# Performance work log

Hardware: AMD Instinct MI355X
Metric: run time of the kernel (lower is better)

## Reference

```python
import jax, jax.numpy as jnp
import numpy as np

ROT_DIM = 32
THETA = 10000.0
HEAD_SIZE = 192


def _rope(t):
    # t: [B, T, D]; rotate first ROT_DIM features with interleaved-pair RoPE
    T = t.shape[1]
    inv_freq = 1.0 / (THETA ** (jnp.arange(0, ROT_DIM, 2, dtype=jnp.float32) / ROT_DIM))  # [16]
    freqs = jnp.arange(T, dtype=jnp.float32)[:, None] * inv_freq[None, :]  # [T,16]
    freqs = jnp.repeat(freqs, 2, axis=-1)  # [T,32], each freq repeated for the pair
    cos = jnp.cos(freqs).astype(t.dtype)
    sin = jnp.sin(freqs).astype(t.dtype)
    x = t[..., :ROT_DIM]
    x1 = x[..., 0::2]
    x2 = x[..., 1::2]
    rot_half = jnp.stack([-x2, x1], axis=-1).reshape(x.shape)  # interleave (-x2, x1)
    rotated = x * cos + rot_half * sin
    return jnp.concatenate([rotated, t[..., ROT_DIM:]], axis=-1)


def setup_inputs() -> dict:
    key = jax.random.key(0)
    k1, k2, k3, k4 = jax.random.split(key, 4)
    B, T, C, H = 64, 512, 768, HEAD_SIZE
    x = jax.random.normal(k1, (B, T, C), dtype=jnp.float32)
    s = 1.0 / np.sqrt(C)
    Wq = jax.random.normal(k2, (C, H), dtype=jnp.float32) * s
    Wk = jax.random.normal(k3, (C, H), dtype=jnp.float32) * s
    Wv = jax.random.normal(k4, (C, H), dtype=jnp.float32) * s
    return {"x": x, "Wq": Wq, "Wk": Wk, "Wv": Wv}


def reference(x, Wq, Wk, Wv):
    B, T, C = x.shape
    q = x @ Wq  # [B,T,H]
    k = x @ Wk
    v = x @ Wv
    q = _rope(q)
    k = _rope(k)
    scale = k.shape[-1] ** -0.5
    scores = jnp.einsum('bqh,bkh->bqk', q, k) * scale  # [B,T,T]
    causal = jnp.tril(jnp.ones((T, T), dtype=bool))
    scores = jnp.where(causal[None, :, :], scores, -jnp.inf)
    weight = jax.nn.softmax(scores, axis=-1)
    # dropout is identity at eval time
    out = jnp.einsum('bqk,bkh->bqh', weight, v)  # [B,T,H]
    return out
```

## Files before the change

### kernel.cpp

```cpp
#include <hip/hip_runtime.h>
#include <cstdint>

typedef __attribute__((ext_vector_type(8))) short short8;
typedef __attribute__((ext_vector_type(4))) float floatx4;

__device__ __forceinline__ unsigned short f2bf(float f) {
  uint32_t u = __builtin_bit_cast(uint32_t, f);
  u += 0x7fffu + ((u >> 16) & 1u);
  return (unsigned short)(u >> 16);
}
__device__ __forceinline__ uint32_t pkbf(float lo, float hi) {
  uint32_t a = __builtin_bit_cast(uint32_t, lo) + 0x8000u;
  uint32_t b = __builtin_bit_cast(uint32_t, hi) + 0x8000u;
  return __builtin_amdgcn_perm(b, a, 0x07060302);
}
__device__ __forceinline__ void gll16(const void* g, void* l) {
  __builtin_amdgcn_global_load_lds(
      (const __attribute__((address_space(1))) unsigned int*)g,
      (__attribute__((address_space(3))) unsigned int*)l, 16, 0, 0);
}

__global__ void prep_w_kernel(const float* __restrict__ Wq,
                              const float* __restrict__ Wk,
                              const float* __restrict__ Wv,
                              unsigned short* __restrict__ Wt) {
  int id = blockIdx.x * 256 + threadIdx.x;
  int bz = id / 18432, rem = id - bz * 18432;
  int kb = rem / 768, s = rem - kb * 768;
  int row = s >> 2, cs = s & 3;
  int c = cs ^ ((row >> 1) & 3);
  const float* W = (bz == 0) ? Wq : (bz == 1) ? Wk : Wv;
  int k0 = kb * 32 + c * 8;
  unsigned short v[8];
#pragma unroll
  for (int e = 0; e < 8; ++e) v[e] = f2bf(W[(size_t)(k0 + e) * 192 + row]);
  uint4 o;
  o.x = v[0] | ((uint32_t)v[1] << 16);
  o.y = v[2] | ((uint32_t)v[3] << 16);
  o.z = v[4] | ((uint32_t)v[5] << 16);
  o.w = v[6] | ((uint32_t)v[7] << 16);
  *(uint4*)(Wt + (size_t)id * 8) = o;
}

__global__ __launch_bounds__(256, 3) void proj_kernel(
    const float* __restrict__ x, const unsigned short* __restrict__ Wt,
    unsigned short* __restrict__ q_ws, unsigned short* __restrict__ k_ws,
    unsigned short* __restrict__ v_ws) {
  __shared__ __align__(16) unsigned short A_lds[3][64 * 32];
  __shared__ __align__(16) unsigned short B_lds[3][192 * 32];
  const int tid = threadIdx.x;
  const int w = tid >> 6, l = tid & 63, quad = l >> 4, ln = l & 15;
  const int wr = w & 1, wc = w >> 1;
  const int m0 = blockIdx.x * 64;
  const int bz = blockIdx.y;

  const int arow = tid >> 2, ac = tid & 3;
  const int aslot = ((ac ^ ((arow >> 1) & 3)) << 4);
  const float* xp = x + (size_t)(m0 + arow) * 768 + ac * 8;
  const unsigned short* wimg = Wt + (size_t)bz * 18432 * 8;

  const int fq = ((quad ^ ((ln >> 1) & 3)) << 4);

  floatx4 acc[2][6];
#pragma unroll
  for (int mi = 0; mi < 2; ++mi)
#pragma unroll
    for (int nj = 0; nj < 6; ++nj) acc[mi][nj] = floatx4{0.f, 0.f, 0.f, 0.f};

  float4 ax0, ay0, ax1, ay1, ax2, ay2;

#define LOADA(S, K0)                               \
  do {                                             \
    ax##S = *(const float4*)(xp + (K0));           \
    ay##S = *(const float4*)(xp + (K0) + 4);       \
  } while (0)
#define STAGEA(S, AB)                                             \
  do {                                                            \
    uint4 ap;                                                     \
    ap.x = pkbf(ax##S.x, ax##S.y);                                \
    ap.y = pkbf(ax##S.z, ax##S.w);                                \
    ap.z = pkbf(ay##S.x, ay##S.y);                                \
    ap.w = pkbf(ay##S.z, ay##S.w);                                \
    *(uint4*)((char*)&A_lds[AB][0] + arow * 64 + aslot) = ap;     \
  } while (0)
#define DMAB(KB1, BB)                                             \
  do {                                                            \
    const unsigned short* src = wimg + (size_t)(KB1)*6144;        \
    char* dstb = (char*)&B_lds[BB][0];                            \
    gll16(src + tid * 8, dstb + tid * 16);                        \
    gll16(src + (256 + tid) * 8, dstb + (256 + tid) * 16);        \
    gll16(src + (512 + tid) * 8, dstb + (512 + tid) * 16);        \
  } while (0)
#define WAITBAR(N)                                                          \
  asm volatile("s_waitcnt vmcnt(" #N ") lgkmcnt(0)\n\ts_barrier" ::: "memory")
#define PCOMPUTE(C)                                                              \
  do {                                                                           \
    short8 af0 = *(const short8*)((const char*)&A_lds[C][0] +                    \
                                  (wr * 32 + ln) * 64 + fq);                     \
    short8 af1 = *(const short8*)((const char*)&A_lds[C][0] +                    \
                                  (wr * 32 + 16 + ln) * 64 + fq);                \
    _Pragma("unroll") for (int nj = 0; nj < 6; ++nj) {                           \
      short8 bf = *(const short8*)((const char*)&B_lds[C][0] +                   \
                                   (wc * 96 + nj * 16 + ln) * 64 + fq);          \
      acc[0][nj] = __builtin_amdgcn_mfma_f32_16x16x32_bf16(af0, bf, acc[0][nj],  \
                                                           0, 0, 0);             \
      acc[1][nj] = __builtin_amdgcn_mfma_f32_16x16x32_bf16(af1, bf, acc[1][nj],  \
                                                           0, 0, 0);             \
    }                                                                            \
  } while (0)
#define BODY(KB, C, P)            \
  do {                            \
    STAGEA(P, P);                 \
    DMAB((KB) + 1, P);            \
    LOADA(C, ((KB) + 3) * 32);    \
    WAITBAR(7);                   \
    PCOMPUTE(C);                  \
  } while (0)

  DMAB(0, 0);
  LOADA(0, 0);
  LOADA(1, 32);
  LOADA(2, 64);
  STAGEA(0, 0);

  BODY(0, 0, 1);
  for (int t = 1; t <= 16; t += 3) {
    BODY(t, 1, 2);
    BODY(t + 1, 2, 0);
    BODY(t + 2, 0, 1);
  }
  BODY(19, 1, 2);
  BODY(20, 2, 0);
  { STAGEA(1, 1); DMAB(22, 1); WAITBAR(5); PCOMPUTE(0); }
  { STAGEA(2, 2); DMAB(23, 2); WAITBAR(3); PCOMPUTE(1); }
  { WAITBAR(0); PCOMPUTE(2); }

#undef LOADA
#undef STAGEA
#undef DMAB
#undef WAITBAR
#undef PCOMPUTE
#undef BODY

  const float R_LG = 0.8304820237218406f;
#define ROPE2(V0, V1, TPOS)                                         \
  do {                                                              \
    float i0 = (float)(ln >> 1);                                    \
    float f0 = exp2f(-i0 * R_LG);                                   \
    float f1 = exp2f(-(i0 + 8.0f) * R_LG);                          \
    float s0, c0, s1, c1;                                           \
    sincosf((float)(TPOS)*f0, &s0, &c0);                            \
    sincosf((float)(TPOS)*f1, &s1, &c1);                            \
    float p0 = __shfl_xor(V0, 1), p1 = __shfl_xor(V1, 1);           \
    V0 = (ln & 1) ? (V0 * c0 + p0 * s0) : (V0 * c0 - p0 * s0);      \
    V1 = (ln & 1) ? (V1 * c1 + p1 * s1) : (V1 * c1 - p1 * s1);      \
  } while (0)

  if (bz < 2) {
    unsigned short* dst = (bz == 0) ? q_ws : k_ws;
    if (wc == 0) {
#pragma unroll
      for (int mi = 0; mi < 2; ++mi)
#pragma unroll
        for (int r = 0; r < 4; ++r) {
          int row_g = m0 + wr * 32 + mi * 16 + quad * 4 + r;
          int t_pos = row_g & 511;
          float v0 = acc[mi][0][r], v1 = acc[mi][1][r];
          ROPE2(v0, v1, t_pos);
          dst[(size_t)row_g * 192 + ln] = f2bf(v0);
          dst[(size_t)row_g * 192 + 16 + ln] = f2bf(v1);
#pragma unroll
          for (int nj = 2; nj < 6; ++nj)
            dst[(size_t)row_g * 192 + nj * 16 + ln] = f2bf(acc[mi][nj][r]);
        }
    } else {
#pragma unroll
      for (int mi = 0; mi < 2; ++mi)
#pragma unroll
        for (int r = 0; r < 4; ++r) {
          int row_g = m0 + wr * 32 + mi * 16 + quad * 4 + r;
#pragma unroll
          for (int nj = 0; nj < 6; ++nj)
            dst[(size_t)row_g * 192 + 96 + nj * 16 + ln] = f2bf(acc[mi][nj][r]);
        }
    }
  } else {
    const int dbase = wc * 96;
#pragma unroll
    for (int mi = 0; mi < 2; ++mi) {
      int rb = m0 + wr * 32 + mi * 16 + quad * 4;
      int bb = rb >> 9, t = rb & 511;
#pragma unroll
      for (int nj = 0; nj < 6; ++nj) {
        ushort4 pv;
        pv.x = f2bf(acc[mi][nj][0]);
        pv.y = f2bf(acc[mi][nj][1]);
        pv.z = f2bf(acc[mi][nj][2]);
        pv.w = f2bf(acc[mi][nj][3]);
        *(ushort4*)&v_ws[((size_t)bb * 192 + dbase + nj * 16 + ln) * 512 + t] = pv;
      }
    }
  }
#undef ROPE2
}

__global__ __launch_bounds__(256) void attn_kernel(
    const unsigned short* __restrict__ q_ws, const unsigned short* __restrict__ k_ws,
    const unsigned short* __restrict__ v_ws, float* __restrict__ out) {
  __shared__ __align__(16) unsigned short K_lds[64 * 200];
  __shared__ __align__(16) unsigned short V_lds[192 * 72];
  __shared__ __align__(16) unsigned short P_lds[4][16 * 72];
  const int tid = threadIdx.x;
  const int w = tid >> 6, l = tid & 63, quad = l >> 4, ln = l & 15;
  const int b = blockIdx.y;
  const int qt = (blockIdx.y < 32) ? blockIdx.x : 7 - blockIdx.x;
  const int q0 = qt * 64;

  short8 qf[6];
  {
    const unsigned short* qp =
        q_ws + (size_t)(b * 512 + q0 + w * 16 + ln) * 192 + quad * 8;
#pragma unroll
    for (int kk = 0; kk < 6; ++kk) qf[kk] = *(const short8*)(qp + kk * 32);
  }

  float m_i[4], l_i[4];
  floatx4 o[12];
#pragma unroll
  for (int r = 0; r < 4; ++r) { m_i[r] = -1e30f; l_i[r] = 0.f; }
#pragma unroll
  for (int nt = 0; nt < 12; ++nt) o[nt] = floatx4{0.f, 0.f, 0.f, 0.f};
  const float sm_scale = 0.07216878364870323f;

  for (int kt = 0; kt <= qt; ++kt) {
    const int k0 = kt * 64;
    __syncthreads();
#pragma unroll
    for (int it = 0; it < 6; ++it) {
      int idx = it * 256 + tid;
      int row = idx / 24, c = idx - row * 24;
      uint4 v = *(const uint4*)(k_ws + (size_t)(b * 512 + k0 + row) * 192 + c * 8);
      *(uint4*)&K_lds[row * 200 + c * 8] = v;
    }
#pragma unroll
    for (int it = 0; it < 6; ++it) {
      int idx = it * 256 + tid;
      int row = idx >> 3, c = idx & 7;
      uint4 v = *(const uint4*)(v_ws + (size_t)(b * 192 + row) * 512 + k0 + c * 8);
      *(uint4*)&V_lds[row * 72 + c * 8] = v;
    }
    __syncthreads();

    float s[4][4];
    __builtin_amdgcn_s_setprio(1);
#pragma unroll
    for (int nt = 0; nt < 4; ++nt) {
      floatx4 sa = floatx4{0.f, 0.f, 0.f, 0.f};
#pragma unroll
      for (int kk = 0; kk < 6; ++kk) {
        short8 kf = *(const short8*)&K_lds[(nt * 16 + ln) * 200 + kk * 32 + quad * 8];
        sa = __builtin_amdgcn_mfma_f32_16x16x32_bf16(qf[kk], kf, sa, 0, 0, 0);
      }
#pragma unroll
      for (int r = 0; r < 4; ++r) s[nt][r] = sa[r] * sm_scale;
    }
    __builtin_amdgcn_s_setprio(0);
    if (kt == qt) {
#pragma unroll
      for (int nt = 0; nt < 4; ++nt)
#pragma unroll
        for (int r = 0; r < 4; ++r)
          if (nt * 16 + ln > w * 16 + quad * 4 + r) s[nt][r] = -1e30f;
    }
    float alpha[4];
#pragma unroll
    for (int r = 0; r < 4; ++r) {
      float mx = fmaxf(fmaxf(s[0][r], s[1][r]), fmaxf(s[2][r], s[3][r]));
      mx = fmaxf(mx, __shfl_xor(mx, 1));
      mx = fmaxf(mx, __shfl_xor(mx, 2));
      mx = fmaxf(mx, __shfl_xor(mx, 4));
      mx = fmaxf(mx, __shfl_xor(mx, 8));
      float mnew = fmaxf(m_i[r], mx);
      alpha[r] = __expf(m_i[r] - mnew);
      float sum = 0.f;
#pragma unroll
      for (int nt = 0; nt < 4; ++nt) {
        s[nt][r] = __expf(s[nt][r] - mnew);
        sum += s[nt][r];
      }
      sum += __shfl_xor(sum, 1);
      sum += __shfl_xor(sum, 2);
      sum += __shfl_xor(sum, 4);
      sum += __shfl_xor(sum, 8);
      l_i[r] = l_i[r] * alpha[r] + sum;
      m_i[r] = mnew;
    }
#pragma unroll
    for (int nt = 0; nt < 12; ++nt)
#pragma unroll
      for (int r = 0; r < 4; ++r) o[nt][r] *= alpha[r];

#pragma unroll
    for (int nt = 0; nt < 4; ++nt)
#pragma unroll
      for (int r = 0; r < 4; ++r)
        P_lds[w][(quad * 4 + r) * 72 + nt * 16 + ln] = f2bf(s[nt][r]);
    __asm__ volatile("s_waitcnt lgkmcnt(0)" ::: "memory");

    __builtin_amdgcn_s_setprio(1);
#pragma unroll
    for (int ks = 0; ks < 2; ++ks) {
      short8 pf = *(const short8*)&P_lds[w][ln * 72 + ks * 32 + quad * 8];
#pragma unroll
      for (int nt = 0; nt < 12; ++nt) {
        short8 vf = *(const short8*)&V_lds[(nt * 16 + ln) * 72 + ks * 32 + quad * 8];
        o[nt] = __builtin_amdgcn_mfma_f32_16x16x32_bf16(pf, vf, o[nt], 0, 0, 0);
      }
    }
    __builtin_amdgcn_s_setprio(0);
  }

#pragma unroll
  for (int r = 0; r < 4; ++r) {
    float inv = 1.0f / l_i[r];
    size_t rowoff = (size_t)(b * 512 + q0 + w * 16 + quad * 4 + r) * 192;
#pragma unroll
    for (int nt = 0; nt < 12; ++nt)
      out[rowoff + nt * 16 + ln] = o[nt][r] * inv;
  }
}

extern "C" void kernel_launch(void* const* d_in, const int* in_sizes, int n_in,
                              void* d_out, int out_size, void* d_ws, size_t ws_size,
                              hipStream_t stream) {
  const float* x = (const float*)d_in[0];
  const float* Wq = (const float*)d_in[1];
  const float* Wk = (const float*)d_in[2];
  const float* Wv = (const float*)d_in[3];
  float* out = (float*)d_out;

  char* ws = (char*)d_ws;
  const size_t QKV_BYTES = (size_t)64 * 512 * 192 * 2;
  unsigned short* q_ws = (unsigned short*)(ws);
  unsigned short* k_ws = (unsigned short*)(ws + QKV_BYTES);
  unsigned short* v_ws = (unsigned short*)(ws + 2 * QKV_BYTES);
  unsigned short* Wt = (unsigned short*)(ws + 3 * QKV_BYTES);

  hipLaunchKernelGGL(prep_w_kernel, dim3(216), dim3(256), 0, stream, Wq, Wk, Wv, Wt);
  hipLaunchKernelGGL(proj_kernel, dim3(512, 3), dim3(256), 0, stream, x, Wt, q_ws, k_ws, v_ws);
  hipLaunchKernelGGL(attn_kernel, dim3(8, 64), dim3(256), 0, stream, q_ws, k_ws, v_ws, out);
}
```

Baseline: 222.5 us.

## Enlarge projection row tile to 128 and shrink attention key tile to 32

The projection GEMM now computes 128 rows per block instead of 64, and each wave covers all 192 output columns. This doubles reuse of each staged weight tile and halves the grid, at the cost of twice as many accumulators and an occupancy hint lowered to 2. The attention kernel now steps through keys in 32-wide tiles, so less work is wasted on fully masked causal blocks, but it runs twice as many loop iterations, each with two block-wide barriers. The pipeline wait counts were adjusted to match the larger A loads.

```diff
diff --git a/kernel.cpp b/kernel.cpp
--- a/kernel.cpp
+++ b/kernel.cpp
@@ -42,46 +42,53 @@
   *(uint4*)(Wt + (size_t)id * 8) = o;
 }
 
-__global__ __launch_bounds__(256, 3) void proj_kernel(
+__global__ __launch_bounds__(256, 2) void proj_kernel(
     const float* __restrict__ x, const unsigned short* __restrict__ Wt,
     unsigned short* __restrict__ q_ws, unsigned short* __restrict__ k_ws,
     unsigned short* __restrict__ v_ws) {
-  __shared__ __align__(16) unsigned short A_lds[3][64 * 32];
+  __shared__ __align__(16) unsigned short A_lds[3][128 * 32];
   __shared__ __align__(16) unsigned short B_lds[3][192 * 32];
   const int tid = threadIdx.x;
   const int w = tid >> 6, l = tid & 63, quad = l >> 4, ln = l & 15;
-  const int wr = w & 1, wc = w >> 1;
-  const int m0 = blockIdx.x * 64;
+  const int m0 = blockIdx.x * 128;
   const int bz = blockIdx.y;
 
   const int arow = tid >> 2, ac = tid & 3;
   const int aslot = ((ac ^ ((arow >> 1) & 3)) << 4);
-  const float* xp = x + (size_t)(m0 + arow) * 768 + ac * 8;
+  const float* xp0 = x + (size_t)(m0 + arow) * 768 + ac * 8;
+  const float* xp1 = xp0 + (size_t)64 * 768;
   const unsigned short* wimg = Wt + (size_t)bz * 18432 * 8;
 
   const int fq = ((quad ^ ((ln >> 1) & 3)) << 4);
 
-  floatx4 acc[2][6];
+  floatx4 acc[2][12];
 #pragma unroll
   for (int mi = 0; mi < 2; ++mi)
 #pragma unroll
-    for (int nj = 0; nj < 6; ++nj) acc[mi][nj] = floatx4{0.f, 0.f, 0.f, 0.f};
-
-  float4 ax0, ay0, ax1, ay1, ax2, ay2;
+    for (int nj = 0; nj < 12; ++nj) acc[mi][nj] = floatx4{0.f, 0.f, 0.f, 0.f};
+
+  float4 a0p, a0q, a0r, a0s, a1p, a1q, a1r, a1s, a2p, a2q, a2r, a2s;
 
 #define LOADA(S, K0)                               \
   do {                                             \
-    ax##S = *(const float4*)(xp + (K0));           \
-    ay##S = *(const float4*)(xp + (K0) + 4);       \
-  } while (0)
-#define STAGEA(S, AB)                                             \
-  do {                                                            \
-    uint4 ap;                                                     \
-    ap.x = pkbf(ax##S.x, ax##S.y);                                \
-    ap.y = pkbf(ax##S.z, ax##S.w);                                \
-    ap.z = pkbf(ay##S.x, ay##S.y);                                \
-    ap.w = pkbf(ay##S.z, ay##S.w);                                \
-    *(uint4*)((char*)&A_lds[AB][0] + arow * 64 + aslot) = ap;     \
+    a##S##p = *(const float4*)(xp0 + (K0));        \
+    a##S##q = *(const float4*)(xp0 + (K0) + 4);    \
+    a##S##r = *(const float4*)(xp1 + (K0));        \
+    a##S##s = *(const float4*)(xp1 + (K0) + 4);    \
+  } while (0)
+#define STAGEA(S, AB)                                                   \
+  do {                                                                  \
+    uint4 ap;                                                           \
+    ap.x = pkbf(a##S##p.x, a##S##p.y);                                  \
+    ap.y = pkbf(a##S##p.z, a##S##p.w);                                  \
+    ap.z = pkbf(a##S##q.x, a##S##q.y);                                  \
+    ap.w = pkbf(a##S##q.z, a##S##q.w);                                  \
+    *(uint4*)((char*)&A_lds[AB][0] + arow * 64 + aslot) = ap;           \
+    ap.x = pkbf(a##S##r.x, a##S##r.y);                                  \
+    ap.y = pkbf(a##S##r.z, a##S##r.w);                                  \
+    ap.z = pkbf(a##S##s.x, a##S##s.y);                                  \
+    ap.w = pkbf(a##S##s.z, a##S##s.w);                                  \
+    *(uint4*)((char*)&A_lds[AB][0] + (arow + 64) * 64 + aslot) = ap;    \
   } while (0)
 #define DMAB(KB1, BB)                                             \
   do {                                                            \
@@ -96,12 +103,12 @@
 #define PCOMPUTE(C)                                                              \
   do {                                                                           \
     short8 af0 = *(const short8*)((const char*)&A_lds[C][0] +                    \
-                                  (wr * 32 + ln) * 64 + fq);                     \
+                                  (w * 32 + ln) * 64 + fq);                      \
     short8 af1 = *(const short8*)((const char*)&A_lds[C][0] +                    \
-                                  (wr * 32 + 16 + ln) * 64 + fq);                \
-    _Pragma("unroll") for (int nj = 0; nj < 6; ++nj) {                           \
+                                  (w * 32 + 16 + ln) * 64 + fq);                 \
+    _Pragma("unroll") for (int nj = 0; nj < 12; ++nj) {                          \
       short8 bf = *(const short8*)((const char*)&B_lds[C][0] +                   \
-                                   (wc * 96 + nj * 16 + ln) * 64 + fq);          \
+                                   (nj * 16 + ln) * 64 + fq);                    \
       acc[0][nj] = __builtin_amdgcn_mfma_f32_16x16x32_bf16(af0, bf, acc[0][nj],  \
                                                            0, 0, 0);             \
       acc[1][nj] = __builtin_amdgcn_mfma_f32_16x16x32_bf16(af1, bf, acc[1][nj],  \
@@ -131,10 +138,9 @@
   }
   BODY(19, 1, 2);
   BODY(20, 2, 0);
-  { STAGEA(1, 1); DMAB(22, 1); WAITBAR(5); PCOMPUTE(0); }
+  { STAGEA(1, 1); DMAB(22, 1); WAITBAR(3); PCOMPUTE(0); }
   { STAGEA(2, 2); DMAB(23, 2); WAITBAR(3); PCOMPUTE(1); }
   { WAITBAR(0); PCOMPUTE(2); }
-
 #undef LOADA
 #undef STAGEA
 #undef DMAB
@@ -143,73 +149,56 @@
 #undef BODY
 
   const float R_LG = 0.8304820237218406f;
-#define ROPE2(V0, V1, TPOS)                                         \
-  do {                                                              \
-    float i0 = (float)(ln >> 1);                                    \
-    float f0 = exp2f(-i0 * R_LG);                                   \
-    float f1 = exp2f(-(i0 + 8.0f) * R_LG);                          \
-    float s0, c0, s1, c1;                                           \
-    sincosf((float)(TPOS)*f0, &s0, &c0);                            \
-    sincosf((float)(TPOS)*f1, &s1, &c1);                            \
-    float p0 = __shfl_xor(V0, 1), p1 = __shfl_xor(V1, 1);           \
-    V0 = (ln & 1) ? (V0 * c0 + p0 * s0) : (V0 * c0 - p0 * s0);      \
-    V1 = (ln & 1) ? (V1 * c1 + p1 * s1) : (V1 * c1 - p1 * s1);      \
-  } while (0)
-
   if (bz < 2) {
     unsigned short* dst = (bz == 0) ? q_ws : k_ws;
-    if (wc == 0) {
-#pragma unroll
-      for (int mi = 0; mi < 2; ++mi)
-#pragma unroll
-        for (int r = 0; r < 4; ++r) {
-          int row_g = m0 + wr * 32 + mi * 16 + quad * 4 + r;
-          int t_pos = row_g & 511;
-          float v0 = acc[mi][0][r], v1 = acc[mi][1][r];
-          ROPE2(v0, v1, t_pos);
-          dst[(size_t)row_g * 192 + ln] = f2bf(v0);
-          dst[(size_t)row_g * 192 + 16 + ln] = f2bf(v1);
-#pragma unroll
-          for (int nj = 2; nj < 6; ++nj)
-            dst[(size_t)row_g * 192 + nj * 16 + ln] = f2bf(acc[mi][nj][r]);
+#pragma unroll
+    for (int mi = 0; mi < 2; ++mi)
+#pragma unroll
+      for (int r = 0; r < 4; ++r) {
+        int row_g = m0 + w * 32 + mi * 16 + quad * 4 + r;
+        int t_pos = row_g & 511;
+        float v0 = acc[mi][0][r], v1 = acc[mi][1][r];
+        {
+          float i0 = (float)(ln >> 1);
+          float f0 = exp2f(-i0 * R_LG);
+          float f1 = exp2f(-(i0 + 8.0f) * R_LG);
+          float s0, c0, s1, c1;
+          sincosf((float)t_pos * f0, &s0, &c0);
+          sincosf((float)t_pos * f1, &s1, &c1);
+          float p0 = __shfl_xor(v0, 1), p1 = __shfl_xor(v1, 1);
+          v0 = (ln & 1) ? (v0 * c0 + p0 * s0) : (v0 * c0 - p0 * s0);
+          v1 = (ln & 1) ? (v1 * c1 + p1 * s1) : (v1 * c1 - p1 * s1);
         }
-    } else {
-#pragma unroll
-      for (int mi = 0; mi < 2; ++mi)
-#pragma unroll
-        for (int r = 0; r < 4; ++r) {
-          int row_g = m0 + wr * 32 + mi * 16 + quad * 4 + r;
-#pragma unroll
-          for (int nj = 0; nj < 6; ++nj)
-            dst[(size_t)row_g * 192 + 96 + nj * 16 + ln] = f2bf(acc[mi][nj][r]);
-        }
-    }
+        dst[(size_t)row_g * 192 + ln] = f2bf(v0);
+        dst[(size_t)row_g * 192 + 16 + ln] = f2bf(v1);
+#pragma unroll
+        for (int nj = 2; nj < 12; ++nj)
+          dst[(size_t)row_g * 192 + nj * 16 + ln] = f2bf(acc[mi][nj][r]);
+      }
   } else {
-    const int dbase = wc * 96;
 #pragma unroll
     for (int mi = 0; mi < 2; ++mi) {
-      int rb = m0 + wr * 32 + mi * 16 + quad * 4;
+      int rb = m0 + w * 32 + mi * 16 + quad * 4;
       int bb = rb >> 9, t = rb & 511;
 #pragma unroll
-      for (int nj = 0; nj < 6; ++nj) {
+      for (int nj = 0; nj < 12; ++nj) {
         ushort4 pv;
         pv.x = f2bf(acc[mi][nj][0]);
         pv.y = f2bf(acc[mi][nj][1]);
         pv.z = f2bf(acc[mi][nj][2]);
         pv.w = f2bf(acc[mi][nj][3]);
-        *(ushort4*)&v_ws[((size_t)bb * 192 + dbase + nj * 16 + ln) * 512 + t] = pv;
-      }
-    }
-  }
-#undef ROPE2
+        *(ushort4*)&v_ws[((size_t)bb * 192 + nj * 16 + ln) * 512 + t] = pv;
+      }
+    }
+  }
 }
 
 __global__ __launch_bounds__(256) void attn_kernel(
     const unsigned short* __restrict__ q_ws, const unsigned short* __restrict__ k_ws,
     const unsigned short* __restrict__ v_ws, float* __restrict__ out) {
-  __shared__ __align__(16) unsigned short K_lds[64 * 200];
-  __shared__ __align__(16) unsigned short V_lds[192 * 72];
-  __shared__ __align__(16) unsigned short P_lds[4][16 * 72];
+  __shared__ __align__(16) unsigned short K_lds[32 * 200];
+  __shared__ __align__(16) unsigned short V_lds[192 * 40];
+  __shared__ __align__(16) unsigned short P_lds[4][16 * 40];
   const int tid = threadIdx.x;
   const int w = tid >> 6, l = tid & 63, quad = l >> 4, ln = l & 15;
   const int b = blockIdx.y;
@@ -232,29 +221,30 @@
   for (int nt = 0; nt < 12; ++nt) o[nt] = floatx4{0.f, 0.f, 0.f, 0.f};
   const float sm_scale = 0.07216878364870323f;
 
-  for (int kt = 0; kt <= qt; ++kt) {
-    const int k0 = kt * 64;
+  const int ktmax = 2 * qt + 1;
+  for (int kt = 0; kt <= ktmax; ++kt) {
+    const int k0 = kt * 32;
     __syncthreads();
 #pragma unroll
-    for (int it = 0; it < 6; ++it) {
+    for (int it = 0; it < 3; ++it) {
       int idx = it * 256 + tid;
       int row = idx / 24, c = idx - row * 24;
       uint4 v = *(const uint4*)(k_ws + (size_t)(b * 512 + k0 + row) * 192 + c * 8);
       *(uint4*)&K_lds[row * 200 + c * 8] = v;
     }
 #pragma unroll
-    for (int it = 0; it < 6; ++it) {
+    for (int it = 0; it < 3; ++it) {
       int idx = it * 256 + tid;
-      int row = idx >> 3, c = idx & 7;
+      int row = idx >> 2, c = idx & 3;
       uint4 v = *(const uint4*)(v_ws + (size_t)(b * 192 + row) * 512 + k0 + c * 8);
-      *(uint4*)&V_lds[row * 72 + c * 8] = v;
+      *(uint4*)&V_lds[row * 40 + c * 8] = v;
     }
     __syncthreads();
 
-    float s[4][4];
+    float s[2][4];
     __builtin_amdgcn_s_setprio(1);
 #pragma unroll
-    for (int nt = 0; nt < 4; ++nt) {
+    for (int nt = 0; nt < 2; ++nt) {
       floatx4 sa = floatx4{0.f, 0.f, 0.f, 0.f};
 #pragma unroll
       for (int kk = 0; kk < 6; ++kk) {
@@ -265,17 +255,18 @@
       for (int r = 0; r < 4; ++r) s[nt][r] = sa[r] * sm_scale;
     }
     __builtin_amdgcn_s_setprio(0);
-    if (kt == qt) {
-#pragma unroll
-      for (int nt = 0; nt < 4; ++nt)
+    if (kt >= 2 * qt) {
+      int kd = (kt - 2 * qt) * 32;
+#pragma unroll
+      for (int nt = 0; nt < 2; ++nt)
 #pragma unroll
         for (int r = 0; r < 4; ++r)
-          if (nt * 16 + ln > w * 16 + quad * 4 + r) s[nt][r] = -1e30f;
+          if (kd + nt * 16 + ln > w * 16 + quad * 4 + r) s[nt][r] = -1e30f;
     }
     float alpha[4];
 #pragma unroll
     for (int r = 0; r < 4; ++r) {
-      float mx = fmaxf(fmaxf(s[0][r], s[1][r]), fmaxf(s[2][r], s[3][r]));
+      float mx = fmaxf(s[0][r], s[1][r]);
       mx = fmaxf(mx, __shfl_xor(mx, 1));
       mx = fmaxf(mx, __shfl_xor(mx, 2));
       mx = fmaxf(mx, __shfl_xor(mx, 4));
@@ -284,7 +275,7 @@
       alpha[r] = __expf(m_i[r] - mnew);
       float sum = 0.f;
 #pragma unroll
-      for (int nt = 0; nt < 4; ++nt) {
+      for (int nt = 0; nt < 2; ++nt) {
         s[nt][r] = __expf(s[nt][r] - mnew);
         sum += s[nt][r];
       }
@@ -301,19 +292,18 @@
       for (int r = 0; r < 4; ++r) o[nt][r] *= alpha[r];
 
 #pragma unroll
-    for (int nt = 0; nt < 4; ++nt)
+    for (int nt = 0; nt < 2; ++nt)
 #pragma unroll
       for (int r = 0; r < 4; ++r)
-        P_lds[w][(quad * 4 + r) * 72 + nt * 16 + ln] = f2bf(s[nt][r]);
+        P_lds[w][(quad * 4 + r) * 40 + nt * 16 + ln] = f2bf(s[nt][r]);
     __asm__ volatile("s_waitcnt lgkmcnt(0)" ::: "memory");
 
     __builtin_amdgcn_s_setprio(1);
-#pragma unroll
-    for (int ks = 0; ks < 2; ++ks) {
-      short8 pf = *(const short8*)&P_lds[w][ln * 72 + ks * 32 + quad * 8];
+    {
+      short8 pf = *(const short8*)&P_lds[w][ln * 40 + quad * 8];
 #pragma unroll
       for (int nt = 0; nt < 12; ++nt) {
-        short8 vf = *(const short8*)&V_lds[(nt * 16 + ln) * 72 + ks * 32 + quad * 8];
+        short8 vf = *(const short8*)&V_lds[(nt * 16 + ln) * 40 + quad * 8];
         o[nt] = __builtin_amdgcn_mfma_f32_16x16x32_bf16(pf, vf, o[nt], 0, 0, 0);
       }
     }
@@ -347,6 +337,6 @@
   unsigned short* Wt = (unsigned short*)(ws + 3 * QKV_BYTES);
 
   hipLaunchKernelGGL(prep_w_kernel, dim3(216), dim3(256), 0, stream, Wq, Wk, Wv, Wt);
-  hipLaunchKernelGGL(proj_kernel, dim3(512, 3), dim3(256), 0, stream, x, Wt, q_ws, k_ws, v_ws);
+  hipLaunchKernelGGL(proj_kernel, dim3(256, 3), dim3(256), 0, stream, x, Wt, q_ws, k_ws, v_ws);
   hipLaunchKernelGGL(attn_kernel, dim3(8, 64), dim3(256), 0, stream, q_ws, k_ws, v_ws, out);
 }
```

Measured after the change: 234.6 us. 1.05x slower.

## Prefetch next K/V tile into registers in attention; reorder projection grid for x reuse

Applied to the files above, without the earlier changes.

The attention loop now issues the global loads for the next K/V tile into registers right after staging the current tile to LDS, so that memory latency overlaps with the QK and PV MFMA work. The projection kernel moves to a flat 1D grid whose block index is remapped so the three Q/K/V projections of the same x row tile run close together, which should improve L2 reuse of x. The prefetch adds 48 VGPRs of double buffers plus a register copy each iteration, which could lower occupancy or cause spills.

```diff
diff --git a/kernel.cpp b/kernel.cpp
--- a/kernel.cpp
+++ b/kernel.cpp
@@ -51,14 +51,16 @@
   const int tid = threadIdx.x;
   const int w = tid >> 6, l = tid & 63, quad = l >> 4, ln = l & 15;
   const int wr = w & 1, wc = w >> 1;
-  const int m0 = blockIdx.x * 64;
-  const int bz = blockIdx.y;
+  const int bid = blockIdx.x;
+  const int x0 = bid & 7, rr = bid >> 3;
+  const int g = rr / 3, bz = rr - g * 3;
+  const int mt = g * 8 + x0;
+  const int m0 = mt * 64;
 
   const int arow = tid >> 2, ac = tid & 3;
   const int aslot = ((ac ^ ((arow >> 1) & 3)) << 4);
   const float* xp = x + (size_t)(m0 + arow) * 768 + ac * 8;
   const unsigned short* wimg = Wt + (size_t)bz * 18432 * 8;
-
   const int fq = ((quad ^ ((ln >> 1) & 3)) << 4);
 
   floatx4 acc[2][6];
@@ -134,7 +136,6 @@
   { STAGEA(1, 1); DMAB(22, 1); WAITBAR(5); PCOMPUTE(0); }
   { STAGEA(2, 2); DMAB(23, 2); WAITBAR(3); PCOMPUTE(1); }
   { WAITBAR(0); PCOMPUTE(2); }
-
 #undef LOADA
 #undef STAGEA
 #undef DMAB
@@ -148,7 +149,7 @@
     float i0 = (float)(ln >> 1);                                    \
     float f0 = exp2f(-i0 * R_LG);                                   \
     float f1 = exp2f(-(i0 + 8.0f) * R_LG);                          \
-    float s0, c0, s1, c1;                                           \
+    float s0, c0, s1, c1;                                            \
     sincosf((float)(TPOS)*f0, &s0, &c0);                            \
     sincosf((float)(TPOS)*f1, &s1, &c1);                            \
     float p0 = __shfl_xor(V0, 1), p1 = __shfl_xor(V1, 1);           \
@@ -232,24 +233,42 @@
   for (int nt = 0; nt < 12; ++nt) o[nt] = floatx4{0.f, 0.f, 0.f, 0.f};
   const float sm_scale = 0.07216878364870323f;
 
+  uint4 kpre0[6], vpre0[6], kpre1[6], vpre1[6];
+
+#define AT_LOAD(KB, VB, K0)                                                        \
+  do {                                                                             \
+    _Pragma("unroll") for (int it = 0; it < 6; ++it) {                             \
+      int idx = it * 256 + tid;                                                    \
+      int row = idx / 24, c = idx - row * 24;                                      \
+      (KB)[it] = *(const uint4*)(k_ws + (size_t)(b * 512 + (K0) + row) * 192 + c * 8); \
+    }                                                                              \
+    _Pragma("unroll") for (int it = 0; it < 6; ++it) {                             \
+      int idx = it * 256 + tid;                                                    \
+      int row = idx >> 3, c = idx & 7;                                             \
+      (VB)[it] = *(const uint4*)(v_ws + (size_t)(b * 192 + row) * 512 + (K0) + c * 8); \
+    }                                                                              \
+  } while (0)
+#define AT_STAGE(KB, VB)                                      \
+  do {                                                        \
+    _Pragma("unroll") for (int it = 0; it < 6; ++it) {        \
+      int idx = it * 256 + tid;                               \
+      int row = idx / 24, c = idx - row * 24;                 \
+      *(uint4*)&K_lds[row * 200 + c * 8] = (KB)[it];          \
+    }                                                         \
+    _Pragma("unroll") for (int it = 0; it < 6; ++it) {        \
+      int idx = it * 256 + tid;                               \
+      int row = idx >> 3, c = idx & 7;                        \
+      *(uint4*)&V_lds[row * 72 + c * 8] = (VB)[it];           \
+    }                                                         \
+  } while (0)
+
+  AT_LOAD(kpre0, vpre0, 0);
+
   for (int kt = 0; kt <= qt; ++kt) {
-    const int k0 = kt * 64;
     __syncthreads();
-#pragma unroll
-    for (int it = 0; it < 6; ++it) {
-      int idx = it * 256 + tid;
-      int row = idx / 24, c = idx - row * 24;
-      uint4 v = *(const uint4*)(k_ws + (size_t)(b * 512 + k0 + row) * 192 + c * 8);
-      *(uint4*)&K_lds[row * 200 + c * 8] = v;
-    }
-#pragma unroll
-    for (int it = 0; it < 6; ++it) {
-      int idx = it * 256 + tid;
-      int row = idx >> 3, c = idx & 7;
-      uint4 v = *(const uint4*)(v_ws + (size_t)(b * 192 + row) * 512 + k0 + c * 8);
-      *(uint4*)&V_lds[row * 72 + c * 8] = v;
-    }
+    AT_STAGE(kpre0, vpre0);
     __syncthreads();
+    if (kt < qt) AT_LOAD(kpre1, vpre1, (kt + 1) * 64);
 
     float s[4][4];
     __builtin_amdgcn_s_setprio(1);
@@ -318,7 +337,16 @@
       }
     }
     __builtin_amdgcn_s_setprio(0);
-  }
+    if (kt < qt) {
+#pragma unroll
+      for (int it = 0; it < 6; ++it) {
+        kpre0[it] = kpre1[it];
+        vpre0[it] = vpre1[it];
+      }
+    }
+  }
+#undef AT_LOAD
+#undef AT_STAGE
 
 #pragma unroll
   for (int r = 0; r < 4; ++r) {
@@ -347,6 +375,6 @@
   unsigned short* Wt = (unsigned short*)(ws + 3 * QKV_BYTES);
 
   hipLaunchKernelGGL(prep_w_kernel, dim3(216), dim3(256), 0, stream, Wq, Wk, Wv, Wt);
-  hipLaunchKernelGGL(proj_kernel, dim3(512, 3), dim3(256), 0, stream, x, Wt, q_ws, k_ws, v_ws);
+  hipLaunchKernelGGL(proj_kernel, dim3(1536), dim3(256), 0, stream, x, Wt, q_ws, k_ws, v_ws);
   hipLaunchKernelGGL(attn_kernel, dim3(8, 64), dim3(256), 0, stream, q_ws, k_ws, v_ws, out);
 }
```

After: 281.2 us. 26.4% more time.
